# Optimization experiments

Hardware: AMD Instinct MI355X
Metric: run time of the kernel (lower is better)

Reference implementation:

```python
import jax, jax.numpy as jnp
import numpy as np

G = 8192          # graphs in batch
A = 5             # num_agents (nodes per graph)
N = G * A         # total nodes
IN_CH = 29
HID = 64
HEADS = 8
D = HID * HEADS   # 512, node/graph feature dim
NOPT = 4
ADIM = 3


def _lin(key, fan_in, fan_out):
    return jax.random.normal(key, (fan_in, fan_out), jnp.float32) / np.sqrt(fan_in)


def setup_inputs() -> dict:
    key = jax.random.key(0)
    ks = jax.random.split(key, 40)
    # --- graph structure: G fully-connected 5-node graphs + self loops ---
    pairs = np.array([(i, j) for i in range(A) for j in range(A) if i != j])  # [20,2]
    base = (np.arange(G)[:, None] * A)
    src = (base + pairs[None, :, 0]).reshape(-1)
    dst = (base + pairs[None, :, 1]).reshape(-1)
    # GATConv adds self loops (fill_value=0.0 for edge_attr)
    loop = np.arange(N)
    edge_src = jnp.asarray(np.concatenate([src, loop]), jnp.int32)
    edge_dst = jnp.asarray(np.concatenate([dst, loop]), jnp.int32)
    e_real = jax.random.uniform(ks[0], (src.shape[0], 1), jnp.float32)
    edge_attr = jnp.concatenate([e_real, jnp.zeros((N, 1), jnp.float32)], axis=0)
    batch_map = jnp.asarray(np.repeat(np.arange(G), A), jnp.int32)
    x = jax.random.normal(ks[1], (N, IN_CH), jnp.float32)
    sc = 1.0 / np.sqrt(HID)
    inp = dict(
        x=x, edge_attr=edge_attr, edge_src=edge_src, edge_dst=edge_dst, batch_map=batch_map,
        # conv1
        W1=_lin(ks[2], IN_CH, D), as1=jax.random.normal(ks[3], (HEADS, HID)) * sc,
        ad1=jax.random.normal(ks[4], (HEADS, HID)) * sc, We1=_lin(ks[5], 1, D),
        ae1=jax.random.normal(ks[6], (HEADS, HID)) * sc, b1=jnp.zeros((D,), jnp.float32),
        # conv2
        W2=_lin(ks[7], D, D), as2=jax.random.normal(ks[8], (HEADS, HID)) * sc,
        ad2=jax.random.normal(ks[9], (HEADS, HID)) * sc, We2=_lin(ks[10], 1, D),
        ae2=jax.random.normal(ks[11], (HEADS, HID)) * sc, b2=jnp.zeros((D,), jnp.float32),
        # policy-over-options head
        pw1=_lin(ks[12], D, 2 * HID), pb1=jnp.zeros((2 * HID,)), pw2=_lin(ks[13], 2 * HID, NOPT), pb2=jnp.zeros((NOPT,)),
        # q-options head
        qw1=_lin(ks[14], D, 2 * HID), qb1=jnp.zeros((2 * HID,)), qw2=_lin(ks[15], 2 * HID, NOPT), qb2=jnp.zeros((NOPT,)),
        # intra-option actor head (option 0), input dim = node + graph feature = 2*D
        aw1=_lin(ks[16], 2 * D, 2 * HID), ab1=jnp.zeros((2 * HID,)), aw2=_lin(ks[17], 2 * HID, 2 * ADIM), ab2=jnp.zeros((2 * ADIM,)),
        # termination head (option 0)
        tw1=_lin(ks[18], D, HID), tb1=jnp.zeros((HID,)), tw2=_lin(ks[19], HID, 1), tb2=jnp.zeros((1,)),
        action_limits=jnp.array([1.0, 1.0, 3.14159], jnp.float32),
    )
    return inp


def _gat(x, src, dst, eattr, W, a_s, a_d, We, a_e, b):
    n = x.shape[0]
    h = (x @ W).reshape(n, HEADS, HID)                      # [N,H,C]
    e = (eattr @ We).reshape(-1, HEADS, HID)                # [E,H,C]
    lg = ((h * a_s).sum(-1)[src] + (h * a_d).sum(-1)[dst]
          + (e * a_e).sum(-1))                              # [E,H]
    lg = jnp.where(lg > 0, lg, 0.2 * lg)                    # leaky_relu(0.2)
    m = jax.ops.segment_max(lg, dst, num_segments=n)
    p = jnp.exp(lg - m[dst])
    denom = jax.ops.segment_sum(p, dst, num_segments=n)[dst] + 1e-16
    alpha = p / denom                                       # scatter-softmax over dst
    out = jax.ops.segment_sum(alpha[:, :, None] * h[src], dst, num_segments=n)
    return out.reshape(n, HEADS * HID) + b


def reference(x, edge_attr, edge_src, edge_dst, batch_map,
              W1, as1, ad1, We1, ae1, b1,
              W2, as2, ad2, We2, ae2, b2,
              pw1, pb1, pw2, pb2, qw1, qb1, qw2, qb2,
              aw1, ab1, aw2, ab2, tw1, tb1, tw2, tb2, action_limits):
    h = jax.nn.relu(_gat(x, edge_src, edge_dst, edge_attr, W1, as1, ad1, We1, ae1, b1))
    h = jax.nn.relu(_gat(h, edge_src, edge_dst, edge_attr, W2, as2, ad2, We2, ae2, b2))
    # global_mean_pool
    cnt = jax.ops.segment_sum(jnp.ones((h.shape[0],), h.dtype), batch_map, num_segments=G)
    g = jax.ops.segment_sum(h, batch_map, num_segments=G) / cnt[:, None]   # [G,D]
    pi = jax.nn.relu(g @ pw1 + pb1) @ pw2 + pb2                            # [G,NOPT]
    q = jax.nn.relu(g @ qw1 + qb1) @ qw2 + qb2                             # [G,NOPT]
    term = jax.nn.sigmoid(jax.nn.relu(g @ tw1 + tb1) @ tw2 + tb2)          # [G,1]
    # per-graph first num_agents nodes == all nodes here (5 per graph)
    agent = h.reshape(G, A, D)
    comb = jnp.concatenate([agent, jnp.broadcast_to(g[:, None, :], (G, A, D))], axis=-1)
    ho = jax.nn.relu(comb @ aw1 + ab1) @ aw2 + ab2                          # [G,A,6]
    mean_raw, log_std_raw = jnp.split(ho, 2, axis=-1)
    mean = jnp.tanh(mean_raw) * action_limits                               # [G,A,3]
    std = 0.05 + jax.nn.sigmoid(log_std_raw) * 0.45 + 1e-6
    return jnp.concatenate([pi, q, term, mean.reshape(G, -1), std.reshape(G, -1)], axis=1)
```

## Files before the change

kernel.cpp:

```cpp
#include <hip/hip_runtime.h>
#include <hip/hip_bf16.h>
#include <math.h>

#define GG 8192
#define AA 5
#define NN (GG * AA)
#define DD 512

typedef unsigned short ushort_t;
typedef unsigned int uint_t;

__device__ inline float bf2f(ushort_t u) {
  union { uint_t i; float f; } c; c.i = ((uint_t)u) << 16; return c.f;
}
__device__ inline ushort_t f2bf(float f) {
  union { float f; uint_t i; } c; c.f = f;
  uint_t r = c.i + 0x7fffu + ((c.i >> 16) & 1u);
  return (ushort_t)(r >> 16);
}

using frag8 = __attribute__((ext_vector_type(8))) short;
using f32x4 = __attribute__((ext_vector_type(4))) float;

typedef __attribute__((address_space(3))) void lds_void;
typedef __attribute__((address_space(1))) const void gbl_void;
#define GLL(g, l) __builtin_amdgcn_global_load_lds((gbl_void*)(g), (lds_void*)(l), 16, 0, 0)

__device__ inline int xcd_swz(int bid, int nwg) {
  return (bid & 7) * (nwg >> 3) + (bid >> 3);
}

__global__ __launch_bounds__(256) void k_prep(
    const float* __restrict__ x, const float* __restrict__ W1,
    const float* __restrict__ W2, const float* __restrict__ pw1,
    const float* __restrict__ qw1, const float* __restrict__ tw1,
    const float* __restrict__ aw1, const float* __restrict__ pb1,
    const float* __restrict__ qb1, const float* __restrict__ tb1,
    const float* __restrict__ ab1, const float* __restrict__ We1,
    const float* __restrict__ ae1, const float* __restrict__ We2,
    const float* __restrict__ ae2, const float* __restrict__ as1,
    const float* __restrict__ ad1, const float* __restrict__ as2,
    const float* __restrict__ ad2, const float* __restrict__ pw2,
    const float* __restrict__ pb2, const float* __restrict__ qw2,
    const float* __restrict__ qb2, const float* __restrict__ tw2,
    const float* __restrict__ tb2, const float* __restrict__ aw2,
    const float* __restrict__ ab2, ushort_t* __restrict__ xpad32,
    ushort_t* __restrict__ W1T32, ushort_t* __restrict__ W2T,
    ushort_t* __restrict__ WcatT, ushort_t* __restrict__ aw1topT,
    ushort_t* __restrict__ wsc1T, ushort_t* __restrict__ wsc2T,
    float* __restrict__ bcat, float* __restrict__ sce,
    float* __restrict__ woutT, float* __restrict__ bout) {
  int b = blockIdx.x;
  int t = threadIdx.x;
  if (b < 1024) {
    int i = b * 256 + t;
    int n = i >> 9, k = i & 511;
    W2T[(size_t)n * 512 + k] = f2bf(W2[(size_t)k * 512 + n]);
    float v;
    if (n < 128)      v = pw1[(size_t)k * 128 + n];
    else if (n < 256) v = qw1[(size_t)k * 128 + (n - 128)];
    else if (n < 320) v = tw1[(size_t)k * 64 + (n - 256)];
    else if (n < 448) v = aw1[(size_t)(512 + k) * 128 + (n - 320)];
    else              v = 0.f;
    WcatT[(size_t)n * 512 + k] = f2bf(v);
    if (n < 128) aw1topT[(size_t)n * 512 + k] = f2bf(aw1[(size_t)k * 128 + n]);
    if (k == 0) {
      float bv;
      if (n < 128)      bv = pb1[n];
      else if (n < 256) bv = qb1[n - 128];
      else if (n < 320) bv = tb1[n - 256];
      else if (n < 448) bv = ab1[n - 320];
      else              bv = 0.f;
      bcat[n] = bv;
    }
    if (i < 512 * 32) {
      int nn = i >> 5, kk = i & 31;
      W1T32[i] = (kk < 29) ? f2bf(W1[(size_t)kk * 512 + nn]) : (ushort_t)0;
    }
    if (i < 8192) {
      int k2 = i & 511, s = i >> 9;
      int head = s >> 1;
      const float* av = ((s & 1) ? ad2 : as2) + head * 64;
      const float* wr = W2 + (size_t)k2 * 512 + head * 64;
      float val = 0.f;
      for (int c = 0; c < 64; ++c) val = fmaf(wr[c], av[c], val);
      wsc2T[i] = f2bf(val);
    }
    if (i < 512) {
      int k1 = i & 31, s = i >> 5;
      int head = s >> 1;
      float val = 0.f;
      if (k1 < 29) {
        const float* av = ((s & 1) ? ad1 : as1) + head * 64;
        const float* wr = W1 + (size_t)k1 * 512 + head * 64;
        for (int c = 0; c < 64; ++c) val = fmaf(wr[c], av[c], val);
      }
      wsc1T[i] = f2bf(val);
    }
    if (i < 16) {
      int h = i & 7;
      const float* Wp = (i < 8) ? We1 : We2;
      const float* ap = (i < 8) ? ae1 : ae2;
      float c = 0.f;
      for (int k2 = 0; k2 < 64; ++k2) c = fmaf(Wp[h * 64 + k2], ap[h * 64 + k2], c);
      sce[i] = c;
    }
    if (i < 5120) {
      int j = i / 40, o = i % 40;
      float wv;
      if (o < 4)       wv = pw2[j * 4 + o];
      else if (o < 8)  wv = qw2[j * 4 + (o - 4)];
      else if (o == 8) wv = (j < 64) ? tw2[j] : 0.f;
      else if (o < 24) wv = aw2[j * 6 + (o - 9) % 3];
      else if (o < 39) wv = aw2[j * 6 + 3 + (o - 24) % 3];
      else             wv = 0.f;
      woutT[i] = wv;
      if (j == 0) {
        float bv;
        if (o < 4)       bv = pb2[o];
        else if (o < 8)  bv = qb2[o - 4];
        else if (o == 8) bv = tb2[0];
        else if (o < 24) bv = ab2[(o - 9) % 3];
        else if (o < 39) bv = ab2[3 + (o - 24) % 3];
        else             bv = 0.f;
        bout[o] = bv;
      }
    }
  } else {
    int i = (b - 1024) * 256 + t;
    int n = i >> 5, k = i & 31;
    xpad32[i] = (k < 29) ? f2bf(x[(size_t)n * 29 + k]) : (ushort_t)0;
  }
}

__global__ __launch_bounds__(1024) void k_mega(
    const ushort_t* __restrict__ xpad32, const ushort_t* __restrict__ W1T32,
    const ushort_t* __restrict__ wsc1T, const ushort_t* __restrict__ W2T,
    const ushort_t* __restrict__ wsc2T, const float* __restrict__ eattr,
    const float* __restrict__ sce, const float* __restrict__ b1,
    const float* __restrict__ b2, ushort_t* __restrict__ h2,
    ushort_t* __restrict__ gmean) {
  __shared__ __align__(16) char smem[149504];
  const int t = threadIdx.x;
  const int lane = t & 63;
  const int w = t >> 6;
  const int l15 = lane & 15;
  const int ko2 = ((((lane >> 4) ^ (lane & 3) ^ ((lane >> 2) & 3)) & 3) * 16);
  int lid = xcd_swz(blockIdx.x, gridDim.x);
  const int m0 = lid * 80;
  const int g0 = lid * 16;
  ushort_t* h1buf = (ushort_t*)smem;
  float* sal = (float*)(smem + 124160);
  float* sss = (float*)(smem + 136960);
  float* ssd = (float*)(smem + 139520);
  const f32x4 zz = {0.f, 0.f, 0.f, 0.f};
  f32x4 acc[5][2], asc[5];
#pragma unroll
  for (int mt = 0; mt < 5; ++mt) { acc[mt][0] = zz; acc[mt][1] = zz; asc[mt] = zz; }

  {
#pragma unroll
    for (int r_ = 0; r_ < 2; ++r_) {
      int c_ = t + r_ * 1024; int row_ = c_ >> 2;
      int sw_ = ((((c_ & 3) ^ (row_ & 3) ^ ((row_ >> 2) & 3)) & 3)) * 8;
      GLL(W1T32 + (size_t)row_ * 32 + sw_, smem + 81920 + c_ * 16);
    }
    if (t < 320) {
      int c_ = t; int row_ = c_ >> 2;
      int sw_ = ((((c_ & 3) ^ (row_ & 3) ^ ((row_ >> 2) & 3)) & 3)) * 8;
      GLL(xpad32 + (size_t)(m0 + row_) * 32 + sw_, smem + 114688 + c_ * 16);
    } else if (t < 384) {
      int c_ = t - 320; int row_ = c_ >> 2;
      int sw_ = ((((c_ & 3) ^ (row_ & 3) ^ ((row_ >> 2) & 3)) & 3)) * 8;
      GLL(wsc1T + (size_t)row_ * 32 + sw_, smem + 119808 + c_ * 16);
    }
  }
  asm volatile("s_waitcnt vmcnt(0)" ::: "memory");
  __builtin_amdgcn_s_barrier();
  {
    const char* bb = smem + 81920;
    const char* aa = smem + 114688;
    const char* sb = smem + 119808;
    frag8 af[5], bfr[2];
#pragma unroll
    for (int mt = 0; mt < 5; ++mt)
      af[mt] = *(const frag8*)(aa + (mt * 16 + l15) * 64 + ko2);
#pragma unroll
    for (int n = 0; n < 2; ++n)
      bfr[n] = *(const frag8*)(bb + ((2 * w + n) * 16 + l15) * 64 + ko2);
#pragma unroll
    for (int mt = 0; mt < 5; ++mt)
#pragma unroll
      for (int n = 0; n < 2; ++n)
        acc[mt][n] = __builtin_amdgcn_mfma_f32_16x16x32_bf16(af[mt], bfr[n], acc[mt][n], 0, 0, 0);
    if (w == 15) {
      frag8 sfr = *(const frag8*)(sb + l15 * 64 + ko2);
#pragma unroll
      for (int mt = 0; mt < 5; ++mt)
        asc[mt] = __builtin_amdgcn_mfma_f32_16x16x32_bf16(af[mt], sfr, asc[mt], 0, 0, 0);
    }
  }
  if (w == 15) {
    float* dst = (l15 & 1) ? ssd : sss;
    int hd = l15 >> 1;
    int q4 = (lane >> 4) * 4;
#pragma unroll
    for (int mt = 0; mt < 5; ++mt)
#pragma unroll
      for (int r = 0; r < 4; ++r)
        dst[(mt * 16 + q4 + r) * 8 + hd] = asc[mt][r];
  }
  __syncthreads();
  if (t < 640) {
    int gi = t / 40, jh = t % 40;
    int j = jh >> 3, hd = jh & 7;
    int g = g0 + gi;
    float sdj = ssd[(gi * 5 + j) * 8 + hd];
    float ce = sce[hd];
    float lg[5], mx = -1e30f;
#pragma unroll
    for (int i = 0; i < 5; ++i) {
      float l = sss[(gi * 5 + i) * 8 + hd] + sdj;
      if (i != j) l = fmaf(eattr[(size_t)g * 20 + i * 4 + (j > i ? j - 1 : j)], ce, l);
      l = l > 0.f ? l : 0.2f * l;
      lg[i] = l; mx = fmaxf(mx, l);
    }
    float s = 0.f;
#pragma unroll
    for (int i = 0; i < 5; ++i) { lg[i] = __expf(lg[i] - mx); s += lg[i]; }
    float inv = 1.f / (s + 1e-16f);
#pragma unroll
    for (int i = 0; i < 5; ++i) sal[((gi * 5 + j) * 5 + i) * 8 + hd] = lg[i] * inv;
  }
  __syncthreads();
  {
    float* hbf = (float*)(smem + 81920);
#pragma unroll
    for (int p = 0; p < 4; ++p) {
      if ((w >> 2) == p) {
        int q4 = (lane >> 4) * 4;
#pragma unroll
        for (int mt = 0; mt < 5; ++mt)
#pragma unroll
          for (int n = 0; n < 2; ++n) {
            int lc = (w & 3) * 32 + n * 16 + l15;
#pragma unroll
            for (int r = 0; r < 4; ++r)
              hbf[(mt * 16 + q4 + r) * 132 + lc] = acc[mt][n][r];
          }
      }
      __syncthreads();
      if (t < 512) {
        int gi = t >> 5, cq = t & 31;
        int hd = 2 * p + (cq >> 4);
        int cg = p * 128 + cq * 4;
        float hv[5][4];
#pragma unroll
        for (int i = 0; i < 5; ++i)
          *(float4*)hv[i] = *(const float4*)&hbf[(gi * 5 + i) * 132 + cq * 4];
        float4 bb4 = *(const float4*)&b1[cg];
        int chunk = cg >> 5, slot = (cg >> 3) & 3, boff = (cg & 7) * 2;
#pragma unroll
        for (int j = 0; j < 5; ++j) {
          float o0 = bb4.x, o1 = bb4.y, o2 = bb4.z, o3 = bb4.w;
#pragma unroll
          for (int i = 0; i < 5; ++i) {
            float a = sal[((gi * 5 + j) * 5 + i) * 8 + hd];
            o0 = fmaf(a, hv[i][0], o0); o1 = fmaf(a, hv[i][1], o1);
            o2 = fmaf(a, hv[i][2], o2); o3 = fmaf(a, hv[i][3], o3);
          }
          o0 = fmaxf(o0, 0.f); o1 = fmaxf(o1, 0.f);
          o2 = fmaxf(o2, 0.f); o3 = fmaxf(o3, 0.f);
          uint2 wv_;
          wv_.x = (uint_t)f2bf(o0) | ((uint_t)f2bf(o1) << 16);
          wv_.y = (uint_t)f2bf(o2) | ((uint_t)f2bf(o3) << 16);
          int row = gi * 5 + j;
          int phys = slot ^ (row & 3) ^ ((row >> 2) & 3);
          *(uint2*)((char*)h1buf + chunk * 5120 + row * 64 + phys * 16 + boff) = wv_;
        }
      }
      __syncthreads();
    }
  }

#pragma unroll
  for (int mt = 0; mt < 5; ++mt) { acc[mt][0] = zz; acc[mt][1] = zz; asc[mt] = zz; }
#define FS2(bi, kk0)                                                           \
  {                                                                            \
    char* bb_ = smem + 81920 + (bi) * 32768;                                   \
    char* sb_ = smem + 147456 + (bi) * 1024;                                   \
    _Pragma("unroll")                                                          \
    for (int r_ = 0; r_ < 2; ++r_) {                                           \
      int c_ = t + r_ * 1024; int row_ = c_ >> 2;                              \
      int sw_ = ((((c_ & 3) ^ (row_ & 3) ^ ((row_ >> 2) & 3)) & 3)) * 8;       \
      GLL(W2T + (size_t)row_ * 512 + (kk0) + sw_, bb_ + c_ * 16);              \
    }                                                                          \
    if (t < 64) {                                                              \
      int c_ = t; int row_ = c_ >> 2;                                          \
      int sw_ = ((((c_ & 3) ^ (row_ & 3) ^ ((row_ >> 2) & 3)) & 3)) * 8;       \
      GLL(wsc2T + (size_t)row_ * 512 + (kk0) + sw_, sb_ + c_ * 16);            \
    }                                                                          \
  }
  FS2(0, 0);
  for (int ts = 0; ts < 16; ++ts) {
    int cur = ts & 1;
    if (ts + 1 < 16) {
      FS2(cur ^ 1, (ts + 1) * 32);
      if (w == 0) { asm volatile("s_waitcnt vmcnt(3)" ::: "memory"); }
      else        { asm volatile("s_waitcnt vmcnt(2)" ::: "memory"); }
    } else {
      asm volatile("s_waitcnt vmcnt(0)" ::: "memory");
    }
    __builtin_amdgcn_s_barrier();
    __builtin_amdgcn_sched_barrier(0);
    const char* bb = smem + 81920 + cur * 32768;
    const char* aa = (const char*)h1buf + ts * 5120;
    const char* sb = smem + 147456 + cur * 1024;
    frag8 af[5], bfr[2];
#pragma unroll
    for (int mt = 0; mt < 5; ++mt)
      af[mt] = *(const frag8*)(aa + (mt * 16 + l15) * 64 + ko2);
#pragma unroll
    for (int n = 0; n < 2; ++n)
      bfr[n] = *(const frag8*)(bb + ((2 * w + n) * 16 + l15) * 64 + ko2);
    __builtin_amdgcn_s_setprio(1);
#pragma unroll
    for (int mt = 0; mt < 5; ++mt)
#pragma unroll
      for (int n = 0; n < 2; ++n)
        acc[mt][n] = __builtin_amdgcn_mfma_f32_16x16x32_bf16(af[mt], bfr[n], acc[mt][n], 0, 0, 0);
    if (w == 15) {
      frag8 sfr = *(const frag8*)(sb + l15 * 64 + ko2);
#pragma unroll
      for (int mt = 0; mt < 5; ++mt)
        asc[mt] = __builtin_amdgcn_mfma_f32_16x16x32_bf16(af[mt], sfr, asc[mt], 0, 0, 0);
    }
    __builtin_amdgcn_s_setprio(0);
    __builtin_amdgcn_sched_barrier(0);
    __builtin_amdgcn_s_barrier();
  }
#undef FS2
  if (w == 15) {
    float* dst = (l15 & 1) ? ssd : sss;
    int hd = l15 >> 1;
    int q4 = (lane >> 4) * 4;
#pragma unroll
    for (int mt = 0; mt < 5; ++mt)
#pragma unroll
      for (int r = 0; r < 4; ++r)
        dst[(mt * 16 + q4 + r) * 8 + hd] = asc[mt][r];
  }
  __syncthreads();
  if (t < 640) {
    int gi = t / 40, jh = t % 40;
    int j = jh >> 3, hd = jh & 7;
    int g = g0 + gi;
    float sdj = ssd[(gi * 5 + j) * 8 + hd];
    float ce = sce[8 + hd];
    float lg[5], mx = -1e30f;
#pragma unroll
    for (int i = 0; i < 5; ++i) {
      float l = sss[(gi * 5 + i) * 8 + hd] + sdj;
      if (i != j) l = fmaf(eattr[(size_t)g * 20 + i * 4 + (j > i ? j - 1 : j)], ce, l);
      l = l > 0.f ? l : 0.2f * l;
      lg[i] = l; mx = fmaxf(mx, l);
    }
    float s = 0.f;
#pragma unroll
    for (int i = 0; i < 5; ++i) { lg[i] = __expf(lg[i] - mx); s += lg[i]; }
    float inv = 1.f / (s + 1e-16f);
#pragma unroll
    for (int i = 0; i < 5; ++i) sal[((gi * 5 + j) * 5 + i) * 8 + hd] = lg[i] * inv;
  }
  __syncthreads();
  {
    float* hbf = (float*)(smem + 81920);
#pragma unroll
    for (int p = 0; p < 4; ++p) {
      if ((w >> 2) == p) {
        int q4 = (lane >> 4) * 4;
#pragma unroll
        for (int mt = 0; mt < 5; ++mt)
#pragma unroll
          for (int n = 0; n < 2; ++n) {
            int lc = (w & 3) * 32 + n * 16 + l15;
#pragma unroll
            for (int r = 0; r < 4; ++r)
              hbf[(mt * 16 + q4 + r) * 132 + lc] = acc[mt][n][r];
          }
      }
      __syncthreads();
      if (t < 512) {
        int gi = t >> 5, cq = t & 31;
        int hd = 2 * p + (cq >> 4);
        int cg = p * 128 + cq * 4;
        float hv[5][4];
#pragma unroll
        for (int i = 0; i < 5; ++i)
          *(float4*)hv[i] = *(const float4*)&hbf[(gi * 5 + i) * 132 + cq * 4];
        float4 bb4 = *(const float4*)&b2[cg];
        float gs0 = 0.f, gs1 = 0.f, gs2 = 0.f, gs3 = 0.f;
#pragma unroll
        for (int j = 0; j < 5; ++j) {
          float o0 = bb4.x, o1 = bb4.y, o2 = bb4.z, o3 = bb4.w;
#pragma unroll
          for (int i = 0; i < 5; ++i) {
            float a = sal[((gi * 5 + j) * 5 + i) * 8 + hd];
            o0 = fmaf(a, hv[i][0], o0); o1 = fmaf(a, hv[i][1], o1);
            o2 = fmaf(a, hv[i][2], o2); o3 = fmaf(a, hv[i][3], o3);
          }
          o0 = fmaxf(o0, 0.f); o1 = fmaxf(o1, 0.f);
          o2 = fmaxf(o2, 0.f); o3 = fmaxf(o3, 0.f);
          uint2 wv_;
          wv_.x = (uint_t)f2bf(o0) | ((uint_t)f2bf(o1) << 16);
          wv_.y = (uint_t)f2bf(o2) | ((uint_t)f2bf(o3) << 16);
          *(uint2*)(h2 + ((size_t)(g0 + gi) * 5 + j) * 512 + cg) = wv_;
          gs0 += o0; gs1 += o1; gs2 += o2; gs3 += o3;
        }
        uint2 wv_;
        wv_.x = (uint_t)f2bf(gs0 * 0.2f) | ((uint_t)f2bf(gs1 * 0.2f) << 16);
        wv_.y = (uint_t)f2bf(gs2 * 0.2f) | ((uint_t)f2bf(gs3 * 0.2f) << 16);
        *(uint2*)(gmean + (size_t)(g0 + gi) * 512 + cg) = wv_;
      }
      __syncthreads();
    }
  }
}

template <int EPI>
__device__ __forceinline__ void gemm_body(
    const ushort_t* __restrict__ A, const ushort_t* __restrict__ BT,
    const float* __restrict__ bias, void* __restrict__ Cv,
    int M, int N, int K, int m0, int n0, char* lds) {
  int t = threadIdx.x;
  int lane = t & 63;
  int wv = t >> 6;
  int wr = (wv >> 1) * 64, wc = (wv & 1) * 64;
  f32x4 acc[4][4] = {};
  int ch0 = t, ch1 = t + 256;
  int row0 = ch0 >> 2, row1 = ch1 >> 2;
  int sw0 = (((ch0 & 3) ^ (row0 & 3) ^ ((row0 >> 2) & 3)) & 3) * 8;
  int sw1 = (((ch1 & 3) ^ (row1 & 3) ^ ((row1 >> 2) & 3)) & 3) * 8;
  int ko2 = ((((lane >> 4) ^ (lane & 3) ^ ((lane >> 2) & 3)) & 3) * 16);
  const int nt = K >> 5;
#define STAGE(bi, kk0)                                                         \
  {                                                                            \
    char* ab = lds + (bi) * 16384;                                             \
    GLL(A + (size_t)(m0 + row0) * K + (kk0) + sw0, ab + ch0 * 16);             \
    GLL(A + (size_t)(m0 + row1) * K + (kk0) + sw1, ab + ch1 * 16);             \
    GLL(BT + (size_t)(n0 + row0) * K + (kk0) + sw0, ab + 8192 + ch0 * 16);     \
    GLL(BT + (size_t)(n0 + row1) * K + (kk0) + sw1, ab + 8192 + ch1 * 16);     \
  }
  STAGE(0, 0);
  if (nt > 1) STAGE(1, 32);
  for (int ts = 0; ts < nt; ++ts) {
    int bi = ts % 3;
    if (ts + 2 < nt) {
      STAGE((ts + 2) % 3, (ts + 2) * 32);
      asm volatile("s_waitcnt vmcnt(8)" ::: "memory");
    } else if (ts + 1 < nt) {
      asm volatile("s_waitcnt vmcnt(4)" ::: "memory");
    } else {
      asm volatile("s_waitcnt vmcnt(0)" ::: "memory");
    }
    __builtin_amdgcn_s_barrier();
    __builtin_amdgcn_sched_barrier(0);
    const char* ab = lds + bi * 16384;
    frag8 af[4], bfr[4];
#pragma unroll
    for (int m = 0; m < 4; ++m)
      af[m] = *(const frag8*)(ab + (wr + m * 16 + (lane & 15)) * 64 + ko2);
#pragma unroll
    for (int n = 0; n < 4; ++n)
      bfr[n] = *(const frag8*)(ab + 8192 + (wc + n * 16 + (lane & 15)) * 64 + ko2);
#pragma unroll
    for (int m = 0; m < 4; ++m)
#pragma unroll
      for (int n = 0; n < 4; ++n)
        acc[m][n] = __builtin_amdgcn_mfma_f32_16x16x32_bf16(af[m], bfr[n], acc[m][n], 0, 0, 0);
    __builtin_amdgcn_sched_barrier(0);
    __builtin_amdgcn_s_barrier();
  }
#undef STAGE
  int r4 = (lane >> 4) * 4;
  int cl = lane & 15;
#pragma unroll
  for (int m = 0; m < 4; ++m) {
#pragma unroll
    for (int n = 0; n < 4; ++n) {
      int col = n0 + wc + n * 16 + cl;
      float bb = (EPI == 2) ? bias[col] : 0.f;
#pragma unroll
      for (int r = 0; r < 4; ++r) {
        int row = m0 + wr + m * 16 + r4 + r;
        float v = acc[m][n][r] + bb;
        if (EPI == 2 && col < 320) v = fmaxf(v, 0.f);
        ((float*)Cv)[(size_t)row * N + col] = v;
      }
    }
  }
}

__global__ __launch_bounds__(256) void k_hgemm(
    const ushort_t* __restrict__ h2, const ushort_t* __restrict__ aw1topT,
    float* __restrict__ ahid, const ushort_t* __restrict__ gmean,
    const ushort_t* __restrict__ WcatT, const float* __restrict__ bcat,
    float* __restrict__ hcat) {
  __shared__ char lds[49152];
  int bid = blockIdx.x;
  if (bid < 320) {
    int lid = xcd_swz(bid, 320);
    gemm_body<1>(h2, aw1topT, nullptr, ahid, NN, 128, DD, lid * 128, 0, lds);
  } else {
    int lid = xcd_swz(bid - 320, 256);
    gemm_body<2>(gmean, WcatT, bcat, hcat, GG, DD, DD, (lid >> 2) * 128, (lid & 3) * 128, lds);
  }
}

__global__ __launch_bounds__(256) void k_heads(
    const float* __restrict__ hcat, const float* __restrict__ ahid,
    const float* __restrict__ woutT, const float* __restrict__ bout,
    const float* __restrict__ alim, float* __restrict__ out) {
  int g0 = blockIdx.x * 4;
  int t = threadIdx.x;
  __shared__ float sbuf[4224];
  for (int i = t; i < 4224; i += 256) {
    int gi = i / 1056, r = i - gi * 1056;
    const float* grow = hcat + (size_t)(g0 + gi) * 512;
    float v = 0.f;
    if (r < 128)                  v = grow[r];
    else if (r >= 132 && r < 260) v = grow[128 + r - 132];
    else if (r >= 264 && r < 328) v = grow[256 + r - 264];
    else if (r >= 396) {
      int q = r - 396; int a = q / 132; int j = q - a * 132;
      if (j < 128)
        v = fmaxf(ahid[((size_t)(g0 + gi) * 5 + a) * 128 + j] + grow[320 + j], 0.f);
    }
    sbuf[i] = v;
  }
  __syncthreads();
  int gi = t >> 6, o = t & 63;
  int oc = o < 39 ? o : 39;
  int seg;
  if (oc < 4)       seg = 0;
  else if (oc < 8)  seg = 132;
  else if (oc == 8) seg = 264;
  else {
    int idx = (oc < 24) ? oc - 9 : oc - 24;
    seg = 396 + (idx / 3) * 132;
  }
  const float* ip = &sbuf[gi * 1056 + seg];
  float a0 = 0.f, a1 = 0.f, a2 = 0.f, a3 = 0.f;
#pragma unroll
  for (int j = 0; j < 128; j += 4) {
    a0 = fmaf(ip[j + 0], woutT[(j + 0) * 40 + oc], a0);
    a1 = fmaf(ip[j + 1], woutT[(j + 1) * 40 + oc], a1);
    a2 = fmaf(ip[j + 2], woutT[(j + 2) * 40 + oc], a2);
    a3 = fmaf(ip[j + 3], woutT[(j + 3) * 40 + oc], a3);
  }
  float res = (a0 + a1) + (a2 + a3) + bout[oc];
  if (o < 39) {
    if (o == 8)       res = 1.f / (1.f + __expf(-res));
    else if (o >= 24) res = 0.05f + 0.45f / (1.f + __expf(-res)) + 1e-6f;
    else if (o >= 9)  res = tanhf(res) * alim[(o - 9) % 3];
    out[(size_t)(g0 + gi) * 39 + o] = res;
  }
}

extern "C" void kernel_launch(void* const* d_in, const int* in_sizes, int n_in,
                              void* d_out, int out_size, void* d_ws, size_t ws_size,
                              hipStream_t stream) {
  const float* x     = (const float*)d_in[0];
  const float* eattr = (const float*)d_in[1];
  const float* W1  = (const float*)d_in[5];
  const float* as1 = (const float*)d_in[6];
  const float* ad1 = (const float*)d_in[7];
  const float* We1 = (const float*)d_in[8];
  const float* ae1 = (const float*)d_in[9];
  const float* b1  = (const float*)d_in[10];
  const float* W2  = (const float*)d_in[11];
  const float* as2 = (const float*)d_in[12];
  const float* ad2 = (const float*)d_in[13];
  const float* We2 = (const float*)d_in[14];
  const float* ae2 = (const float*)d_in[15];
  const float* b2  = (const float*)d_in[16];
  const float* pw1 = (const float*)d_in[17];
  const float* pb1 = (const float*)d_in[18];
  const float* pw2 = (const float*)d_in[19];
  const float* pb2 = (const float*)d_in[20];
  const float* qw1 = (const float*)d_in[21];
  const float* qb1 = (const float*)d_in[22];
  const float* qw2 = (const float*)d_in[23];
  const float* qb2 = (const float*)d_in[24];
  const float* aw1 = (const float*)d_in[25];
  const float* ab1 = (const float*)d_in[26];
  const float* aw2 = (const float*)d_in[27];
  const float* ab2 = (const float*)d_in[28];
  const float* tw1 = (const float*)d_in[29];
  const float* tb1 = (const float*)d_in[30];
  const float* tw2 = (const float*)d_in[31];
  const float* tb2 = (const float*)d_in[32];
  const float* alim = (const float*)d_in[33];

  const size_t BIGE = (size_t)NN * DD;
  char* p = (char*)d_ws;
  ushort_t* h2     = (ushort_t*)p; p += BIGE * 2;
  ushort_t* gmean  = (ushort_t*)p; p += (size_t)GG * DD * 2;
  ushort_t* xpad32 = (ushort_t*)p; p += (size_t)NN * 32 * 2;
  ushort_t* W1T32  = (ushort_t*)p; p += (size_t)512 * 32 * 2;
  ushort_t* W2T    = (ushort_t*)p; p += (size_t)512 * 512 * 2;
  ushort_t* WcatT  = (ushort_t*)p; p += (size_t)512 * 512 * 2;
  ushort_t* aw1topT = (ushort_t*)p; p += (size_t)128 * 512 * 2;
  ushort_t* wsc1T  = (ushort_t*)p; p += (size_t)16 * 32 * 2;
  ushort_t* wsc2T  = (ushort_t*)p; p += (size_t)16 * 512 * 2;
  float* bcat  = (float*)p; p += 512 * 4;
  float* sce   = (float*)p; p += 16 * 4;
  float* woutT = (float*)p; p += 5120 * 4;
  float* bout  = (float*)p; p += 40 * 4;
  float* ahid  = (float*)p; p += (size_t)NN * 128 * 4;
  float* hcat  = (float*)p;

  k_prep<<<1024 + 5120, 256, 0, stream>>>(
      x, W1, W2, pw1, qw1, tw1, aw1, pb1, qb1, tb1, ab1,
      We1, ae1, We2, ae2, as1, ad1, as2, ad2,
      pw2, pb2, qw2, qb2, tw2, tb2, aw2, ab2,
      xpad32, W1T32, W2T, WcatT, aw1topT, wsc1T, wsc2T,
      bcat, sce, woutT, bout);
  k_mega<<<GG / 16, 1024, 0, stream>>>(
      xpad32, W1T32, wsc1T, W2T, wsc2T, eattr, sce, b1, b2, h2, gmean);
  k_hgemm<<<320 + 256, 256, 0, stream>>>(h2, aw1topT, ahid, gmean, WcatT, bcat, hcat);
  k_heads<<<GG / 4, 256, 0, stream>>>(hcat, ahid, woutT, bout, alim, (float*)d_out);
}
```

Before: 111.9 us.

## Load conv2 weight fragments directly from global into registers, dropping LDS staging

The second GAT GEMM no longer stages W2T and wsc2T tiles through double-buffered LDS with global-to-LDS loads and two block barriers per k-step. Each wave now reads its own B fragments straight from global memory into registers, with a two-deep register prefetch, since waves never shared B columns. This removes 32 block-wide barriers and the LDS write/read round trip, and shrinks shared memory. In exchange, each wave is exposed to global/L2 latency, hidden only by register prefetch, and register pressure goes up.

```diff
diff --git a/kernel.cpp b/kernel.cpp
--- a/kernel.cpp
+++ b/kernel.cpp
@@ -140,7 +140,7 @@
     const float* __restrict__ sce, const float* __restrict__ b1,
     const float* __restrict__ b2, ushort_t* __restrict__ h2,
     ushort_t* __restrict__ gmean) {
-  __shared__ __align__(16) char smem[149504];
+  __shared__ __align__(16) char smem[142336];
   const int t = threadIdx.x;
   const int lane = t & 63;
   const int w = t >> 6;
@@ -285,61 +285,70 @@
 
 #pragma unroll
   for (int mt = 0; mt < 5; ++mt) { acc[mt][0] = zz; acc[mt][1] = zz; asc[mt] = zz; }
-#define FS2(bi, kk0)                                                           \
-  {                                                                            \
-    char* bb_ = smem + 81920 + (bi) * 32768;                                   \
-    char* sb_ = smem + 147456 + (bi) * 1024;                                   \
-    _Pragma("unroll")                                                          \
-    for (int r_ = 0; r_ < 2; ++r_) {                                           \
-      int c_ = t + r_ * 1024; int row_ = c_ >> 2;                              \
-      int sw_ = ((((c_ & 3) ^ (row_ & 3) ^ ((row_ >> 2) & 3)) & 3)) * 8;       \
-      GLL(W2T + (size_t)row_ * 512 + (kk0) + sw_, bb_ + c_ * 16);              \
-    }                                                                          \
-    if (t < 64) {                                                              \
-      int c_ = t; int row_ = c_ >> 2;                                          \
-      int sw_ = ((((c_ & 3) ^ (row_ & 3) ^ ((row_ >> 2) & 3)) & 3)) * 8;       \
-      GLL(wsc2T + (size_t)row_ * 512 + (kk0) + sw_, sb_ + c_ * 16);            \
-    }                                                                          \
-  }
-  FS2(0, 0);
-  for (int ts = 0; ts < 16; ++ts) {
-    int cur = ts & 1;
-    if (ts + 1 < 16) {
-      FS2(cur ^ 1, (ts + 1) * 32);
-      if (w == 0) { asm volatile("s_waitcnt vmcnt(3)" ::: "memory"); }
-      else        { asm volatile("s_waitcnt vmcnt(2)" ::: "memory"); }
-    } else {
-      asm volatile("s_waitcnt vmcnt(0)" ::: "memory");
-    }
-    __builtin_amdgcn_s_barrier();
-    __builtin_amdgcn_sched_barrier(0);
-    const char* bb = smem + 81920 + cur * 32768;
-    const char* aa = (const char*)h1buf + ts * 5120;
-    const char* sb = smem + 147456 + cur * 1024;
-    frag8 af[5], bfr[2];
-#pragma unroll
-    for (int mt = 0; mt < 5; ++mt)
-      af[mt] = *(const frag8*)(aa + (mt * 16 + l15) * 64 + ko2);
-#pragma unroll
-    for (int n = 0; n < 2; ++n)
-      bfr[n] = *(const frag8*)(bb + ((2 * w + n) * 16 + l15) * 64 + ko2);
-    __builtin_amdgcn_s_setprio(1);
-#pragma unroll
-    for (int mt = 0; mt < 5; ++mt)
-#pragma unroll
-      for (int n = 0; n < 2; ++n)
-        acc[mt][n] = __builtin_amdgcn_mfma_f32_16x16x32_bf16(af[mt], bfr[n], acc[mt][n], 0, 0, 0);
-    if (w == 15) {
-      frag8 sfr = *(const frag8*)(sb + l15 * 64 + ko2);
-#pragma unroll
-      for (int mt = 0; mt < 5; ++mt)
-        asc[mt] = __builtin_amdgcn_mfma_f32_16x16x32_bf16(af[mt], sfr, asc[mt], 0, 0, 0);
-    }
-    __builtin_amdgcn_s_setprio(0);
-    __builtin_amdgcn_sched_barrier(0);
-    __builtin_amdgcn_s_barrier();
-  }
-#undef FS2
+  {
+    const ushort_t* wB0 = W2T + ((size_t)(2 * w + 0) * 16 + l15) * 512 + (lane >> 4) * 8;
+    const ushort_t* wB1 = W2T + ((size_t)(2 * w + 1) * 16 + l15) * 512 + (lane >> 4) * 8;
+    const ushort_t* wS  = wsc2T + (size_t)l15 * 512 + (lane >> 4) * 8;
+    frag8 pbA0 = *(const frag8*)(wB0);
+    frag8 pbA1 = *(const frag8*)(wB1);
+    frag8 pbB0 = *(const frag8*)(wB0 + 32);
+    frag8 pbB1 = *(const frag8*)(wB1 + 32);
+    frag8 psA = {}, psB = {};
+    if (w == 15) { psA = *(const frag8*)(wS); psB = *(const frag8*)(wS + 32); }
+#pragma unroll
+    for (int ts = 0; ts < 16; ts += 2) {
+      {
+        frag8 c0 = pbA0, c1 = pbA1, cs = psA;
+        if (ts + 2 < 16) {
+          pbA0 = *(const frag8*)(wB0 + (ts + 2) * 32);
+          pbA1 = *(const frag8*)(wB1 + (ts + 2) * 32);
+          if (w == 15) psA = *(const frag8*)(wS + (ts + 2) * 32);
+        }
+        const char* aa = (const char*)h1buf + ts * 5120;
+        frag8 af[5];
+#pragma unroll
+        for (int mt = 0; mt < 5; ++mt)
+          af[mt] = *(const frag8*)(aa + (mt * 16 + l15) * 64 + ko2);
+        __builtin_amdgcn_s_setprio(1);
+#pragma unroll
+        for (int mt = 0; mt < 5; ++mt) {
+          acc[mt][0] = __builtin_amdgcn_mfma_f32_16x16x32_bf16(af[mt], c0, acc[mt][0], 0, 0, 0);
+          acc[mt][1] = __builtin_amdgcn_mfma_f32_16x16x32_bf16(af[mt], c1, acc[mt][1], 0, 0, 0);
+        }
+        if (w == 15) {
+#pragma unroll
+          for (int mt = 0; mt < 5; ++mt)
+            asc[mt] = __builtin_amdgcn_mfma_f32_16x16x32_bf16(af[mt], cs, asc[mt], 0, 0, 0);
+        }
+        __builtin_amdgcn_s_setprio(0);
+      }
+      {
+        frag8 c0 = pbB0, c1 = pbB1, cs = psB;
+        if (ts + 3 < 16) {
+          pbB0 = *(const frag8*)(wB0 + (ts + 3) * 32);
+          pbB1 = *(const frag8*)(wB1 + (ts + 3) * 32);
+          if (w == 15) psB = *(const frag8*)(wS + (ts + 3) * 32);
+        }
+        const char* aa = (const char*)h1buf + (ts + 1) * 5120;
+        frag8 af[5];
+#pragma unroll
+        for (int mt = 0; mt < 5; ++mt)
+          af[mt] = *(const frag8*)(aa + (mt * 16 + l15) * 64 + ko2);
+        __builtin_amdgcn_s_setprio(1);
+#pragma unroll
+        for (int mt = 0; mt < 5; ++mt) {
+          acc[mt][0] = __builtin_amdgcn_mfma_f32_16x16x32_bf16(af[mt], c0, acc[mt][0], 0, 0, 0);
+          acc[mt][1] = __builtin_amdgcn_mfma_f32_16x16x32_bf16(af[mt], c1, acc[mt][1], 0, 0, 0);
+        }
+        if (w == 15) {
+#pragma unroll
+          for (int mt = 0; mt < 5; ++mt)
+            asc[mt] = __builtin_amdgcn_mfma_f32_16x16x32_bf16(af[mt], cs, asc[mt], 0, 0, 0);
+        }
+        __builtin_amdgcn_s_setprio(0);
+      }
+    }
+  }
   if (w == 15) {
     float* dst = (l15 & 1) ? ssd : sss;
     int hd = l15 >> 1;
```

New measurement: 161.6 us. 44.3% more time.
